# Performance work log

Hardware: AMD Instinct MI355X
Metric: run time of the kernel (lower is better)

Reference implementation:

```python
import jax, jax.numpy as jnp
import numpy as np

B, SEQ, PRED, N, PATCH, STRIDE = 4, 720, 720, 64, 16, 8
DM, EL = 256, 2
PNUM = (PRED + SEQ - PATCH) // STRIDE + 2  # 180
EPS = 1e-5


def _gelu(x):
    return jax.nn.gelu(x, approximate=False)  # torch nn.GELU default (erf)


def _ln(x, w, b):
    mu = x.mean(-1, keepdims=True)
    var = ((x - mu) ** 2).mean(-1, keepdims=True)
    return (x - mu) / jnp.sqrt(var + EPS) * w + b


def _pos_emb(n, d):
    pos = np.arange(n)[:, None].astype(np.float32)
    div = np.exp(np.arange(0, d, 2).astype(np.float32) * (-np.log(10000.0) / d))
    pe = np.zeros((n, d), np.float32)
    pe[:, 0::2] = np.sin(pos * div)
    pe[:, 1::2] = np.cos(pos * div)
    return jnp.asarray(pe)


def _patch_embed(x, emb_w):
    # x: [B, N, L]; ReplicationPad1d((0, STRIDE)) then unfold(patch_len, stride)
    xp = jnp.concatenate([x, jnp.repeat(x[..., -1:], STRIDE, axis=-1)], axis=-1)
    npatch = (xp.shape[-1] - PATCH) // STRIDE + 1
    idx = jnp.arange(npatch)[:, None] * STRIDE + jnp.arange(PATCH)[None, :]
    patches = xp[..., idx]  # [B, N, npatch, PATCH]
    emb = jnp.einsum('bnpl,ld->bnpd', patches, emb_w) + _pos_emb(npatch, DM)
    return emb.reshape(-1, npatch, DM)  # [B*N, npatch, DM]


def _temp_mix(x, w1, b1, w2, b2, nw, nb):
    # Pnum independent Linear(DM,DM)->GELU->Linear(DM,DM), residual + LayerNorm
    h = _gelu(jnp.einsum('bpd,pde->bpe', x, w1) + b1[None])
    o = jnp.einsum('bpd,pde->bpe', h, w2) + b2[None]
    return _ln(o + x, nw, nb)


def _chan_mix(x, w1, b1, w2, b2, nw, nb):
    # DM independent Linear(PNUM,PNUM)->GELU->Linear(PNUM,PNUM), residual + LayerNorm
    h = _gelu(jnp.einsum('bpd,dpq->bqd', x, w1) + b1.T[None])
    o = jnp.einsum('bpd,dpq->bqd', h, w2) + b2.T[None]
    return _ln(o + x, nw, nb)


def _s_correction(x, x_pre):
    xf = jnp.fft.rfft(x, axis=1, norm='ortho')
    pf = jnp.fft.rfft(x_pre, axis=1, norm='ortho')
    xi = jnp.maximum(jnp.fft.irfft(xf * jnp.conj(xf), axis=1), 0.0)
    pi = jnp.maximum(jnp.fft.irfft(pf * jnp.conj(pf), axis=1), 0.0)
    alpha = (xi * pi).sum(1, keepdims=True) / ((pi * pi).sum(1, keepdims=True) + 0.001)
    return jnp.sqrt(alpha)


def _forward(history_data, future_data, revin_w, revin_b, pred_w, pred_b, emb_w,
             ln_w, ln_b, comb_w, comb_b, head_w, head_b,
             tmd_w1, tmd_b1, tmd_w2, tmd_b2, tmd_nw, tmd_nb,
             cmd_w1, cmd_b1, cmd_w2, cmd_b2, cmd_nw, cmd_nb,
             tmu_w1, tmu_b1, tmu_w2, tmu_b2, tmu_nw, tmu_nb,
             cmu_w1, cmu_b1, cmu_w2, cmu_b2, cmu_nw, cmu_nb):
    x0 = history_data[:, :, :, 0]  # [B, SEQ, N]
    mean = x0.mean(1, keepdims=True)
    stdev = jnp.sqrt(x0.var(1, keepdims=True) + EPS)  # unbiased=False
    xn = (x0 - mean) / stdev * revin_w + revin_b  # RevIN norm (affine)
    x = jnp.einsum('bln,lt->bnt', xn, pred_w) + pred_b  # predict_linear on [B,N,SEQ]
    xi = _patch_embed(x, emb_w)  # [B*N, PNUM, DM]
    x_old = _patch_embed(jnp.transpose(x0, (0, 2, 1)), emb_w)  # [B*N, P_old, DM]
    x_all = jnp.zeros(xi.shape + (EL,), xi.dtype)
    for li in range(EL):
        xud = _temp_mix(xi, tmd_w1[li], tmd_b1[li], tmd_w2[li], tmd_b2[li], tmd_nw[li], tmd_nb[li])
        xud = _chan_mix(xud, cmd_w1[li], cmd_b1[li], cmd_w2[li], cmd_b2[li], cmd_nw[li], cmd_nb[li])
        for j in range(li, -1, -1):
            xud = _temp_mix(xud, tmu_w1[j], tmu_b1[j], tmu_w2[j], tmu_b2[j], tmu_nw[j], tmu_nb[j])
            xud = _chan_mix(xud, cmu_w1[j], cmu_b1[j], cmu_w2[j], cmu_b2[j], cmu_nw[j], cmu_nb[j])
        # faithful to original: inner loop shadows `i`, so the write index is always 0
        x_all = x_all.at[:, :, :, 0].set(xud)
    xc = jnp.einsum('bpde,e->bpd', x_all, comb_w) + comb_b  # comb: Linear(EL, 1)
    p_old = x_old.shape[1]
    xc = _s_correction(_ln(x_old, ln_w, ln_b), _ln(xc[:, :p_old, :], ln_w, ln_b)) * xc
    xr = xc.reshape(-1, N, PNUM, DM).transpose(0, 1, 3, 2)  # [B, N, DM, PNUM]
    out = xr.reshape(xr.shape[0], N, DM * PNUM) @ head_w + head_b  # Flatten_Head -> [B, N, PRED]
    out = jnp.transpose(out, (0, 2, 1))  # [B, PRED, N]
    out = (out - revin_b) / (revin_w + EPS * EPS) * stdev + mean  # RevIN denorm
    return out[:, -PRED:, :][..., None]  # [B, PRED, N, 1]


def setup_inputs() -> dict:
    key = jax.random.key(0)
    ks = iter(jax.random.split(key, 64))
    f = lambda shape, s=0.02: s * jax.random.normal(next(ks), shape, jnp.float32)
    inp = dict(
        history_data=jax.random.normal(next(ks), (B, SEQ, N, 1), jnp.float32),
        future_data=jax.random.normal(next(ks), (B, PRED, N, 1), jnp.float32),
        batch_seen=0, epoch=0, train=0,
        revin_w=jnp.ones((N,), jnp.float32), revin_b=jnp.zeros((N,), jnp.float32),
        pred_w=f((SEQ, SEQ + PRED)), pred_b=jnp.zeros((SEQ + PRED,), jnp.float32),
        emb_w=f((PATCH, DM)),
        ln_w=jnp.ones((DM,), jnp.float32), ln_b=jnp.zeros((DM,), jnp.float32),
        comb_w=f((EL,), 0.5), comb_b=jnp.zeros((), jnp.float32),
        head_w=f((DM * PNUM, PRED), 0.005), head_b=jnp.zeros((PRED,), jnp.float32),
    )
    for pre in ('tmd', 'tmu'):
        inp[pre + '_w1'] = f((EL, PNUM, DM, DM)); inp[pre + '_b1'] = jnp.zeros((EL, PNUM, DM), jnp.float32)
        inp[pre + '_w2'] = f((EL, PNUM, DM, DM)); inp[pre + '_b2'] = jnp.zeros((EL, PNUM, DM), jnp.float32)
        inp[pre + '_nw'] = jnp.ones((EL, DM), jnp.float32); inp[pre + '_nb'] = jnp.zeros((EL, DM), jnp.float32)
    for pre in ('cmd', 'cmu'):
        inp[pre + '_w1'] = f((EL, DM, PNUM, PNUM)); inp[pre + '_b1'] = jnp.zeros((EL, DM, PNUM), jnp.float32)
        inp[pre + '_w2'] = f((EL, DM, PNUM, PNUM)); inp[pre + '_b2'] = jnp.zeros((EL, DM, PNUM), jnp.float32)
        inp[pre + '_nw'] = jnp.ones((EL, DM), jnp.float32); inp[pre + '_nb'] = jnp.zeros((EL, DM), jnp.float32)
    return inp


def reference(history_data, future_data, revin_w, revin_b, pred_w, pred_b, emb_w,
              ln_w, ln_b, comb_w, comb_b, head_w, head_b,
              tmd_w1, tmd_b1, tmd_w2, tmd_b2, tmd_nw, tmd_nb,
              cmd_w1, cmd_b1, cmd_w2, cmd_b2, cmd_nw, cmd_nb,
              tmu_w1, tmu_b1, tmu_w2, tmu_b2, tmu_nw, tmu_nb,
              cmu_w1, cmu_b1, cmu_w2, cmu_b2, cmu_nw, cmu_nb,
              batch_seen, epoch, train):
    return _forward(history_data, future_data, revin_w, revin_b, pred_w, pred_b, emb_w,
                    ln_w, ln_b, comb_w, comb_b, head_w, head_b,
                    tmd_w1, tmd_b1, tmd_w2, tmd_b2, tmd_nw, tmd_nb,
                    cmd_w1, cmd_b1, cmd_w2, cmd_b2, cmd_nw, cmd_nb,
                    tmu_w1, tmu_b1, tmu_w2, tmu_b2, tmu_nw, tmu_nb,
                    cmu_w1, cmu_b1, cmu_w2, cmu_b2, cmu_nw, cmu_nb)
```

## Files before the change

### kernel.cpp

```cpp
#include <hip/hip_runtime.h>
#include <cstdint>
#include <cstddef>

namespace {

constexpr int SEQ_ = 720;
constexpr int N_ = 64;
constexpr int T_ = 1440;
constexpr int P_ = 180;
constexpr int PO_ = 90;
constexpr int D_ = 256;
constexpr int PD_ = P_ * D_;
constexpr float EPS_ = 1e-5f;

typedef __attribute__((ext_vector_type(8))) short bf16x8;
typedef __attribute__((ext_vector_type(4))) float f32x4;
typedef __attribute__((ext_vector_type(4))) unsigned short u16x4;

__device__ __forceinline__ float gelu_exact(float x) {
  return 0.5f * x * (1.0f + erff(x * 0.70710678118654752f));
}

__device__ __forceinline__ unsigned short f2bf(float x) {
  unsigned int u = __float_as_uint(x);
  u += 0x7FFFu + ((u >> 16) & 1u);
  return (unsigned short)(u >> 16);
}

__device__ __forceinline__ float bf2f(unsigned short h) {
  return __uint_as_float(((unsigned int)h) << 16);
}

__global__ __launch_bounds__(256) void revin_stats_kernel(
    const float* __restrict__ hist, const float* __restrict__ rw,
    const float* __restrict__ rb, float* __restrict__ meanA,
    float* __restrict__ stdevA, float* __restrict__ sA, float* __restrict__ sB) {
  int b = blockIdx.x;
  int tid = threadIdx.x;
  int n = tid & 63, c = tid >> 6;
  float s = 0.f, s2 = 0.f;
  for (int l = c; l < SEQ_; l += 4) {
    float v = hist[(size_t)(b * SEQ_ + l) * N_ + n];
    s += v; s2 += v * v;
  }
  __shared__ float rs[4][64], rq[4][64];
  rs[c][n] = s; rq[c][n] = s2;
  __syncthreads();
  if (tid < 64) {
    float S = rs[0][tid] + rs[1][tid] + rs[2][tid] + rs[3][tid];
    float Q = rq[0][tid] + rq[1][tid] + rq[2][tid] + rq[3][tid];
    float mu = S * (1.f / (float)SEQ_);
    float var = Q * (1.f / (float)SEQ_) - mu * mu;
    float sd = sqrtf(var + EPS_);
    int bn = b * 64 + tid;
    meanA[bn] = mu; stdevA[bn] = sd;
    float a = rw[tid] / sd;
    sA[bn] = a;
    sB[bn] = rb[tid] - mu * a;
  }
}

__global__ __launch_bounds__(256) void pred_kernel(
    const float* __restrict__ hist, const float* __restrict__ predw,
    const float* __restrict__ predb, const float* __restrict__ sA,
    const float* __restrict__ sB, float* __restrict__ xbuf) {
  int b = blockIdx.y;
  int t = blockIdx.x * 32 + (threadIdx.x & 31);
  int ng = threadIdx.x >> 5;
  const float* hb = hist + (size_t)b * SEQ_ * N_ + ng * 8;
  float acc[8] = {0.f,0.f,0.f,0.f,0.f,0.f,0.f,0.f};
  float wsum = 0.f;
  #pragma unroll 4
  for (int l = 0; l < SEQ_; l++) {
    float w = predw[(size_t)l * T_ + t];
    float4 h0 = *reinterpret_cast<const float4*>(hb + (size_t)l * N_);
    float4 h1 = *reinterpret_cast<const float4*>(hb + (size_t)l * N_ + 4);
    acc[0] += h0.x * w; acc[1] += h0.y * w; acc[2] += h0.z * w; acc[3] += h0.w * w;
    acc[4] += h1.x * w; acc[5] += h1.y * w; acc[6] += h1.z * w; acc[7] += h1.w * w;
    wsum += w;
  }
  float pb = predb[t];
  #pragma unroll
  for (int q = 0; q < 8; q++) {
    int bn = b * 64 + ng * 8 + q;
    xbuf[(size_t)bn * T_ + t] = sA[bn] * acc[q] + sB[bn] * wsum + pb;
  }
}

__global__ __launch_bounds__(256) void embed_kernel(
    const float* __restrict__ src, const float* __restrict__ embw,
    unsigned short* __restrict__ dst, int mode,
    float* __restrict__ muX, float* __restrict__ rsX) {
  __shared__ float Es[16 * 256];
  __shared__ float Ss[128];
  __shared__ float pS[15][4], pQ[15][4];
  int bn = blockIdx.y;
  int p0 = blockIdx.x * 15;
  int tid = threadIdx.x;
  for (int i = tid; i < 16 * 256; i += 256) Es[i] = embw[i];
  if (tid < 128) {
    int t = p0 * 8 + tid;
    float v;
    if (mode == 0) {
      int tc = t < T_ ? t : (T_ - 1);
      v = src[(size_t)bn * T_ + tc];
    } else {
      int tc = t < SEQ_ ? t : (SEQ_ - 1);
      int b = bn >> 6, n = bn & 63;
      v = src[(size_t)(b * SEQ_ + tc) * N_ + n];
    }
    Ss[tid] = v;
  }
  __syncthreads();
  int np = (mode == 0) ? P_ : PO_;
  float dv = expf(-0.035977892078032f * (float)(tid & ~1));
  int w = tid >> 6, l = tid & 63;
  for (int pi = 0; pi < 15; pi++) {
    int p = p0 + pi;
    float acc = 0.f;
    #pragma unroll
    for (int k = 0; k < 16; k++) acc += Ss[pi * 8 + k] * Es[k * 256 + tid];
    float ang = (float)p * dv;
    float pe = (tid & 1) ? cosf(ang) : sinf(ang);
    float ov = acc + pe;
    dst[((size_t)bn * np + p) * D_ + tid] = f2bf(ov);
    if (mode == 1) {
      float s = ov, q = ov * ov;
      #pragma unroll
      for (int off = 32; off > 0; off >>= 1) { s += __shfl_xor(s, off); q += __shfl_xor(q, off); }
      if (l == 0) { pS[pi][w] = s; pQ[pi][w] = q; }
    }
  }
  if (mode == 1) {
    __syncthreads();
    if (tid < 15) {
      float S = pS[tid][0] + pS[tid][1] + pS[tid][2] + pS[tid][3];
      float Q = pQ[tid][0] + pQ[tid][1] + pQ[tid][2] + pQ[tid][3];
      float mu = S * (1.f / 256.f);
      int idx = bn * 90 + p0 + tid;
      muX[idx] = mu;
      rsX[idx] = rsqrtf(Q * (1.f / 256.f) - mu * mu + EPS_);
    }
  }
}

struct TileInfo {
  const float* Wg; unsigned short* Og;
  int K, Nn, Kp, k0, n0;
};

__device__ __forceinline__ TileInfo decode_tile(
    int bid,
    const float* t0, const float* t1, const float* t2, const float* t3,
    const float* t4, const float* t5,
    const float* c0, const float* c1, const float* c2, const float* c3,
    const float* c4p, const float* c5, const float* hw,
    unsigned short* WtAll, unsigned short* WcAll, unsigned short* WhAll) {
  TileInfo ti;
  int tk, tn;
  if (bid < 17280) {
    int tt = bid / 2880, rem = bid - tt * 2880;
    int g = rem >> 4, tile = rem & 15;
    const float* s = t0;
    if (tt == 1) s = t1; else if (tt == 2) s = t2; else if (tt == 3) s = t3;
    else if (tt == 4) s = t4; else if (tt == 5) s = t5;
    ti.Wg = s + (size_t)g * 65536;
    ti.Og = WtAll + (size_t)tt * 11796480 + (size_t)g * 65536;
    ti.K = 256; ti.Nn = 256; ti.Kp = 256; tk = tile >> 2; tn = tile & 3;
  } else if (bid < 31104) {
    int b2 = bid - 17280;
    int tt = b2 / 2304, rem = b2 - tt * 2304;
    int g = rem / 9, tile = rem - g * 9;
    const float* s = c0;
    if (tt == 1) s = c1; else if (tt == 2) s = c2; else if (tt == 3) s = c3;
    else if (tt == 4) s = c4p; else if (tt == 5) s = c5;
    ti.Wg = s + (size_t)g * 32400;
    ti.Og = WcAll + (size_t)tt * 9437184 + (size_t)g * 36864;
    ti.K = 180; ti.Nn = 180; ti.Kp = 192; tk = tile / 3; tn = tile - (tile / 3) * 3;
  } else {
    int b2 = bid - 31104;
    ti.Wg = hw; ti.Og = WhAll;
    ti.K = 46080; ti.Nn = 720; ti.Kp = 46080; tk = b2 / 12; tn = b2 - (b2 / 12) * 12;
  }
  ti.k0 = tk * 64; ti.n0 = tn * 64;
  return ti;
}

__global__ __launch_bounds__(256) void convT_all_kernel(
    const float* t0, const float* t1, const float* t2, const float* t3,
    const float* t4, const float* t5,
    const float* c0, const float* c1, const float* c2, const float* c3,
    const float* c4p, const float* c5,
    const float* hw,
    unsigned short* WtAll, unsigned short* WcAll, unsigned short* WhAll,
    int tbase, int tcount) {
  __shared__ float Ts[2][64][65];
  int tid = threadIdx.x;
  int kr = tid >> 4, nc = (tid & 15) * 4;
  int G = gridDim.x;
  int tend = tbase + tcount;

  auto do_load = [&](const TileInfo& ti, float4* r) {
    #pragma unroll
    for (int i = 0; i < 4; i++) {
      int k = ti.k0 + kr + i * 16;
      float4 v = make_float4(0.f, 0.f, 0.f, 0.f);
      if (k < ti.K) {
        int n = ti.n0 + nc;
        if (n + 3 < ti.Nn) {
          v = *reinterpret_cast<const float4*>(ti.Wg + (size_t)k * ti.Nn + n);
        } else {
          if (n + 0 < ti.Nn) v.x = ti.Wg[(size_t)k * ti.Nn + n + 0];
          if (n + 1 < ti.Nn) v.y = ti.Wg[(size_t)k * ti.Nn + n + 1];
          if (n + 2 < ti.Nn) v.z = ti.Wg[(size_t)k * ti.Nn + n + 2];
          if (n + 3 < ti.Nn) v.w = ti.Wg[(size_t)k * ti.Nn + n + 3];
        }
      }
      r[i] = v;
    }
  };

  auto do_write = [&](const float4* r, int b) {
    #pragma unroll
    for (int i = 0; i < 4; i++) {
      Ts[b][kr + i * 16][nc + 0] = r[i].x;
      Ts[b][kr + i * 16][nc + 1] = r[i].y;
      Ts[b][kr + i * 16][nc + 2] = r[i].z;
      Ts[b][kr + i * 16][nc + 3] = r[i].w;
    }
  };

  auto do_store = [&](const TileInfo& ti, int b) {
    #pragma unroll
    for (int it = 0; it < 2; it++) {
      int nr = (tid >> 3) + it * 32;
      int kc = (tid & 7) * 8;
      unsigned int tmp[4];
      #pragma unroll
      for (int j = 0; j < 4; j++) {
        unsigned int lo = f2bf(Ts[b][kc + 2 * j][nr]);
        unsigned int hi = f2bf(Ts[b][kc + 2 * j + 1][nr]);
        tmp[j] = lo | (hi << 16);
      }
      uint4 vv; vv.x = tmp[0]; vv.y = tmp[1]; vv.z = tmp[2]; vv.w = tmp[3];
      *reinterpret_cast<uint4*>(ti.Og + (size_t)(ti.n0 + nr) * ti.Kp + ti.k0 + kc) = vv;
    }
  };

#define DECODE(tt) decode_tile((tt), t0,t1,t2,t3,t4,t5, c0,c1,c2,c3,c4p,c5, hw, WtAll, WcAll, WhAll)

  int t = tbase + blockIdx.x;
  if (t >= tend) return;

  float4 rA[4], rB[4];
  TileInfo i0 = DECODE(t);
  do_load(i0, rA);
  bool v1 = (t + G < tend);
  TileInfo i1 = v1 ? DECODE(t + G) : i0;
  if (v1) do_load(i1, rB);
  do_write(rA, 0);
  bool v2 = (t + 2 * G < tend);
  TileInfo i2 = v2 ? DECODE(t + 2 * G) : i0;
  if (v2) do_load(i2, rA);
  __syncthreads();

  while (true) {
    if (v1) do_write(rB, 1);
    {
      bool v3 = (t + 3 * G < tend);
      TileInfo i3 = i2;
      if (v3) { i3 = DECODE(t + 3 * G); do_load(i3, rB); }
      do_store(i0, 0);
      __syncthreads();
      t += G;
      if (!v1) return;
      i0 = i1; i1 = i2; i2 = i3; v1 = v2; v2 = v3;
    }
    if (v1) do_write(rA, 0);
    {
      bool v3 = (t + 3 * G < tend);
      TileInfo i3 = i2;
      if (v3) { i3 = DECODE(t + 3 * G); do_load(i3, rA); }
      do_store(i0, 1);
      __syncthreads();
      t += G;
      if (!v1) return;
      i0 = i1; i1 = i2; i2 = i3; v1 = v2; v2 = v3;
    }
  }
#undef DECODE
}

__global__ __launch_bounds__(256, 2) void temp_mfma_kernel(
    const unsigned short* __restrict__ X, unsigned short* __restrict__ Y,
    const unsigned short* __restrict__ W1t, const float* __restrict__ B1,
    const unsigned short* __restrict__ W2t, const float* __restrict__ B2,
    const float* __restrict__ NW, const float* __restrict__ NB) {
  __shared__ __align__(16) short Xs[64 * 256];
  __shared__ __align__(16) short Hs[64 * 256];
  __shared__ float partS[64][4];
  __shared__ float partQ[64][4];
  int lin = (blockIdx.x & 7) * 90 + (blockIdx.x >> 3);
  int p = lin >> 2;
  int m0 = (lin & 3) << 6;
  int tid = threadIdx.x;
  int w = tid >> 6, l = tid & 63;
  int lr = l & 15, lq = l >> 4;

  const unsigned short* Xblk = X + (size_t)m0 * PD_ + (size_t)p * D_;
  for (int i = tid; i < 64 * 32; i += 256) {
    int r = i >> 5, c8 = (i & 31) << 3;
    uint4 v = *reinterpret_cast<const uint4*>(Xblk + (size_t)r * PD_ + c8);
    *reinterpret_cast<uint4*>(&Xs[r * 256 + (c8 ^ ((r & 7) << 3))]) = v;
  }
  __syncthreads();

  int n0w = w << 6;
  f32x4 zero4 = {0.f, 0.f, 0.f, 0.f};
  f32x4 acc[4][4];
  #pragma unroll
  for (int a = 0; a < 4; a++)
    #pragma unroll
    for (int b = 0; b < 4; b++) acc[a][b] = zero4;

  const unsigned short* W1p = W1t + (size_t)p * 65536;
  {
    bf16x8 bhc[4], bhn[4];
    #pragma unroll
    for (int nf = 0; nf < 4; nf++)
      bhc[nf] = *reinterpret_cast<const bf16x8*>(W1p + (size_t)(n0w + nf * 16 + lr) * 256 + lq * 8);
    for (int ks = 0; ks < 8; ks++) {
      int kb = ks * 32 + lq * 8;
      bf16x8 af[4];
      #pragma unroll
      for (int mf = 0; mf < 4; mf++) {
        int r = mf * 16 + lr;
        af[mf] = *reinterpret_cast<const bf16x8*>(&Xs[r * 256 + (kb ^ ((r & 7) << 3))]);
      }
      if (ks < 7) {
        #pragma unroll
        for (int nf = 0; nf < 4; nf++)
          bhn[nf] = *reinterpret_cast<const bf16x8*>(W1p + (size_t)(n0w + nf * 16 + lr) * 256 + kb + 32);
      }
      #pragma unroll
      for (int mf = 0; mf < 4; mf++)
        #pragma unroll
        for (int nf = 0; nf < 4; nf++)
          acc[mf][nf] = __builtin_amdgcn_mfma_f32_16x16x32_bf16(af[mf], bhc[nf], acc[mf][nf], 0, 0, 0);
      if (ks < 7) {
        #pragma unroll
        for (int nf = 0; nf < 4; nf++) bhc[nf] = bhn[nf];
      }
    }
  }

  #pragma unroll
  for (int nf = 0; nf < 4; nf++) {
    int n = n0w + nf * 16 + lr;
    float bias = B1[p * 256 + n];
    #pragma unroll
    for (int mf = 0; mf < 4; mf++)
      #pragma unroll
      for (int rg = 0; rg < 4; rg++) {
        int r = mf * 16 + lq * 4 + rg;
        Hs[r * 256 + (n ^ ((r & 7) << 3))] =
            (short)f2bf(gelu_exact(acc[mf][nf][rg] + bias));
      }
  }
  __syncthreads();

  #pragma unroll
  for (int a = 0; a < 4; a++)
    #pragma unroll
    for (int b = 0; b < 4; b++) acc[a][b] = zero4;
  const unsigned short* W2p = W2t + (size_t)p * 65536;
  {
    bf16x8 bhc[4], bhn[4];
    #pragma unroll
    for (int nf = 0; nf < 4; nf++)
      bhc[nf] = *reinterpret_cast<const bf16x8*>(W2p + (size_t)(n0w + nf * 16 + lr) * 256 + lq * 8);
    for (int ks = 0; ks < 8; ks++) {
      int kb = ks * 32 + lq * 8;
      bf16x8 af[4];
      #pragma unroll
      for (int mf = 0; mf < 4; mf++) {
        int r = mf * 16 + lr;
        af[mf] = *reinterpret_cast<const bf16x8*>(&Hs[r * 256 + (kb ^ ((r & 7) << 3))]);
      }
      if (ks < 7) {
        #pragma unroll
        for (int nf = 0; nf < 4; nf++)
          bhn[nf] = *reinterpret_cast<const bf16x8*>(W2p + (size_t)(n0w + nf * 16 + lr) * 256 + kb + 32);
      }
      #pragma unroll
      for (int mf = 0; mf < 4; mf++)
        #pragma unroll
        for (int nf = 0; nf < 4; nf++)
          acc[mf][nf] = __builtin_amdgcn_mfma_f32_16x16x32_bf16(af[mf], bhc[nf], acc[mf][nf], 0, 0, 0);
      if (ks < 7) {
        #pragma unroll
        for (int nf = 0; nf < 4; nf++) bhc[nf] = bhn[nf];
      }
    }
  }

  float b2v[4], nwv[4], nbv[4];
  #pragma unroll
  for (int nf = 0; nf < 4; nf++) {
    int n = n0w + nf * 16 + lr;
    b2v[nf] = B2[p * 256 + n];
    nwv[nf] = NW[n];
    nbv[nf] = NB[n];
  }
  #pragma unroll
  for (int nf = 0; nf < 4; nf++) {
    int n = n0w + nf * 16 + lr;
    #pragma unroll
    for (int mf = 0; mf < 4; mf++)
      #pragma unroll
      for (int rg = 0; rg < 4; rg++) {
        int r = mf * 16 + lq * 4 + rg;
        float res = bf2f((unsigned short)Xs[r * 256 + (n ^ ((r & 7) << 3))]);
        acc[mf][nf][rg] += b2v[nf] + res;
      }
  }
  #pragma unroll
  for (int mf = 0; mf < 4; mf++)
    #pragma unroll
    for (int rg = 0; rg < 4; rg++) {
      float s = acc[mf][0][rg] + acc[mf][1][rg] + acc[mf][2][rg] + acc[mf][3][rg];
      float q = acc[mf][0][rg] * acc[mf][0][rg] + acc[mf][1][rg] * acc[mf][1][rg] +
                acc[mf][2][rg] * acc[mf][2][rg] + acc[mf][3][rg] * acc[mf][3][rg];
      #pragma unroll
      for (int off = 1; off < 16; off <<= 1) {
        s += __shfl_xor(s, off);
        q += __shfl_xor(q, off);
      }
      if (lr == 0) {
        int r = mf * 16 + lq * 4 + rg;
        partS[r][w] = s;
        partQ[r][w] = q;
      }
    }
  __syncthreads();
  #pragma unroll
  for (int mf = 0; mf < 4; mf++)
    #pragma unroll
    for (int rg = 0; rg < 4; rg++) {
      int r = mf * 16 + lq * 4 + rg;
      float S = partS[r][0] + partS[r][1] + partS[r][2] + partS[r][3];
      float Q = partQ[r][0] + partQ[r][1] + partQ[r][2] + partQ[r][3];
      float mu = S * (1.f / 256.f);
      float rstd = rsqrtf(Q * (1.f / 256.f) - mu * mu + EPS_);
      #pragma unroll
      for (int nf = 0; nf < 4; nf++) {
        int n = n0w + nf * 16 + lr;
        Hs[r * 256 + (n ^ ((r & 7) << 3))] =
            (short)f2bf((acc[mf][nf][rg] - mu) * rstd * nwv[nf] + nbv[nf]);
      }
    }
  __syncthreads();
  unsigned short* Yblk = Y + (size_t)m0 * PD_ + (size_t)p * D_;
  for (int i = tid; i < 64 * 32; i += 256) {
    int r = i >> 5, c8 = (i & 31) << 3;
    uint4 v = *reinterpret_cast<uint4*>(&Hs[r * 256 + (c8 ^ ((r & 7) << 3))]);
    *reinterpret_cast<uint4*>(Yblk + (size_t)r * PD_ + c8) = v;
  }
}

__global__ __launch_bounds__(256) void tr_AB_kernel(
    const unsigned short* __restrict__ A, unsigned short* __restrict__ B16) {
  __shared__ unsigned short T[32][184];
  int bn = blockIdx.y;
  int d0 = blockIdx.x * 32;
  int tid = threadIdx.x;
  int ld = tid & 31, pw = tid >> 5;
  for (int p = pw; p < 180; p += 8)
    T[ld][p] = A[((size_t)bn * 180 + p) * 256 + d0 + ld];
  __syncthreads();
  unsigned int* Bu = reinterpret_cast<unsigned int*>(B16);
  for (int i = tid; i < 32 * 96; i += 256) {
    int r = i / 96, jj = i - r * 96;
    int p0 = 2 * jj;
    unsigned int lo = (p0 < 180) ? (unsigned int)T[r][p0] : 0u;
    unsigned int hi = (p0 + 1 < 180) ? (unsigned int)T[r][p0 + 1] : 0u;
    Bu[((size_t)bn * 256 + d0 + r) * 96 + jj] = lo | (hi << 16);
  }
}

__global__ __launch_bounds__(256, 2) void chan_mfma_kernel(
    const unsigned short* __restrict__ Xb, unsigned short* __restrict__ Yb,
    const unsigned short* __restrict__ W1t, const float* __restrict__ B1,
    const unsigned short* __restrict__ W2t, const float* __restrict__ B2) {
  __shared__ __align__(16) short Xs[64 * 200];
  __shared__ __align__(16) short Hs[64 * 200];
  int lin = (blockIdx.x & 7) * 128 + (blockIdx.x >> 3);
  int d = lin >> 2;
  int m0 = (lin & 3) << 6;
  int tid = threadIdx.x;
  int w = tid >> 6, l = tid & 63;
  int lr = l & 15, lq = l >> 4;

  for (int i = tid; i < 64 * 24; i += 256) {
    int r = i / 24, c = i - r * 24;
    uint4 v = *reinterpret_cast<const uint4*>(
        Xb + ((size_t)(m0 + r) * 256 + d) * 192 + c * 8);
    *reinterpret_cast<uint4*>(&Xs[r * 200 + c * 8]) = v;
  }
  __syncthreads();

  int n0w = w * 48;
  f32x4 zero4 = {0.f, 0.f, 0.f, 0.f};
  f32x4 acc[4][3];
  #pragma unroll
  for (int a = 0; a < 4; a++)
    #pragma unroll
    for (int b = 0; b < 3; b++) acc[a][b] = zero4;

  const unsigned short* W1p = W1t + (size_t)d * (192 * 192);
  {
    bf16x8 bhc[3], bhn[3];
    #pragma unroll
    for (int nf = 0; nf < 3; nf++)
      bhc[nf] = *reinterpret_cast<const bf16x8*>(W1p + (size_t)(n0w + nf * 16 + lr) * 192 + lq * 8);
    for (int ks = 0; ks < 6; ks++) {
      int kb = ks * 32 + lq * 8;
      bf16x8 af[4];
      #pragma unroll
      for (int mf = 0; mf < 4; mf++)
        af[mf] = *reinterpret_cast<const bf16x8*>(&Xs[(mf * 16 + lr) * 200 + kb]);
      if (ks < 5) {
        #pragma unroll
        for (int nf = 0; nf < 3; nf++)
          bhn[nf] = *reinterpret_cast<const bf16x8*>(W1p + (size_t)(n0w + nf * 16 + lr) * 192 + kb + 32);
      }
      #pragma unroll
      for (int mf = 0; mf < 4; mf++)
        #pragma unroll
        for (int nf = 0; nf < 3; nf++)
          acc[mf][nf] = __builtin_amdgcn_mfma_f32_16x16x32_bf16(af[mf], bhc[nf], acc[mf][nf], 0, 0, 0);
      if (ks < 5) {
        #pragma unroll
        for (int nf = 0; nf < 3; nf++) bhc[nf] = bhn[nf];
      }
    }
  }

  #pragma unroll
  for (int nf = 0; nf < 3; nf++) {
    int n = n0w + nf * 16 + lr;
    bool valid = n < 180;
    float bias = valid ? B1[d * 180 + n] : 0.f;
    #pragma unroll
    for (int mf = 0; mf < 4; mf++)
      #pragma unroll
      for (int rg = 0; rg < 4; rg++) {
        int r = mf * 16 + lq * 4 + rg;
        float h = valid ? gelu_exact(acc[mf][nf][rg] + bias) : 0.f;
        Hs[r * 200 + n] = (short)f2bf(h);
      }
  }
  __syncthreads();

  #pragma unroll
  for (int a = 0; a < 4; a++)
    #pragma unroll
    for (int b = 0; b < 3; b++) acc[a][b] = zero4;
  const unsigned short* W2p = W2t + (size_t)d * (192 * 192);
  {
    bf16x8 bhc[3], bhn[3];
    #pragma unroll
    for (int nf = 0; nf < 3; nf++)
      bhc[nf] = *reinterpret_cast<const bf16x8*>(W2p + (size_t)(n0w + nf * 16 + lr) * 192 + lq * 8);
    for (int ks = 0; ks < 6; ks++) {
      int kb = ks * 32 + lq * 8;
      bf16x8 af[4];
      #pragma unroll
      for (int mf = 0; mf < 4; mf++)
        af[mf] = *reinterpret_cast<const bf16x8*>(&Hs[(mf * 16 + lr) * 200 + kb]);
      if (ks < 5) {
        #pragma unroll
        for (int nf = 0; nf < 3; nf++)
          bhn[nf] = *reinterpret_cast<const bf16x8*>(W2p + (size_t)(n0w + nf * 16 + lr) * 192 + kb + 32);
      }
      #pragma unroll
      for (int mf = 0; mf < 4; mf++)
        #pragma unroll
        for (int nf = 0; nf < 3; nf++)
          acc[mf][nf] = __builtin_amdgcn_mfma_f32_16x16x32_bf16(af[mf], bhc[nf], acc[mf][nf], 0, 0, 0);
      if (ks < 5) {
        #pragma unroll
        for (int nf = 0; nf < 3; nf++) bhc[nf] = bhn[nf];
      }
    }
  }

  #pragma unroll
  for (int nf = 0; nf < 3; nf++) {
    int n = n0w + nf * 16 + lr;
    if (n < 180) {
      float b2v = B2[d * 180 + n];
      #pragma unroll
      for (int mf = 0; mf < 4; mf++)
        #pragma unroll
        for (int rg = 0; rg < 4; rg++) {
          int r = mf * 16 + lq * 4 + rg;
          float res = bf2f((unsigned short)Xs[r * 200 + n]);
          Yb[((size_t)(m0 + r) * 256 + d) * 180 + n] = f2bf(acc[mf][nf][rg] + b2v + res);
        }
    }
  }
}

__global__ __launch_bounds__(256) void trLN_kernel(
    const unsigned short* __restrict__ Bsrc, unsigned short* __restrict__ A,
    const float* __restrict__ nw, const float* __restrict__ nb,
    const float* __restrict__ cw, const float* __restrict__ cb, int useComb,
    float* __restrict__ muP, float* __restrict__ rsP) {
  __shared__ float Tl[16][260];
  int bn = blockIdx.y;
  int p0 = blockIdx.x * 16;
  int tid = threadIdx.x;
  int j = tid & 15, db = tid >> 4;
  #pragma unroll 4
  for (int it = 0; it < 16; ++it) {
    int dd = it * 16 + db;
    float v = 0.f;
    if (p0 + j < 180)
      v = bf2f(Bsrc[((size_t)(bn * 256) + dd) * 180 + p0 + j]);
    Tl[j][dd] = v;
  }
  __syncthreads();
  int w = tid >> 6, l = tid & 63;
  float scale = 1.f, shift = 0.f;
  if (useComb) { scale = cw[0]; shift = cb[0]; }
  float4 w4 = *reinterpret_cast<const float4*>(nw + l * 4);
  float4 b4 = *reinterpret_cast<const float4*>(nb + l * 4);
  #pragma unroll
  for (int rr = 0; rr < 4; ++rr) {
    int row = w * 4 + rr;
    int p = p0 + row;
    float4 v = *reinterpret_cast<const float4*>(&Tl[row][l * 4]);
    float s = v.x + v.y + v.z + v.w;
    float s2 = v.x*v.x + v.y*v.y + v.z*v.z + v.w*v.w;
    #pragma unroll
    for (int off = 32; off > 0; off >>= 1) { s += __shfl_xor(s, off); s2 += __shfl_xor(s2, off); }
    float mu = s * (1.f/256.f);
    float rstd = rsqrtf(s2 * (1.f/256.f) - mu * mu + EPS_);
    if (p < 180) {
      float o0 = ((v.x - mu) * rstd * w4.x + b4.x) * scale + shift;
      float o1 = ((v.y - mu) * rstd * w4.y + b4.y) * scale + shift;
      float o2 = ((v.z - mu) * rstd * w4.z + b4.z) * scale + shift;
      float o3 = ((v.w - mu) * rstd * w4.w + b4.w) * scale + shift;
      unsigned int w0 = (unsigned int)f2bf(o0) | ((unsigned int)f2bf(o1) << 16);
      unsigned int w1 = (unsigned int)f2bf(o2) | ((unsigned int)f2bf(o3) << 16);
      unsigned int* dst = reinterpret_cast<unsigned int*>(
          A + ((size_t)bn * 180 + p) * 256 + l * 4);
      dst[0] = w0; dst[1] = w1;
      if (useComb && p < 90) {
        float so = o0 + o1 + o2 + o3;
        float qo = o0*o0 + o1*o1 + o2*o2 + o3*o3;
        #pragma unroll
        for (int off = 32; off > 0; off >>= 1) { so += __shfl_xor(so, off); qo += __shfl_xor(qo, off); }
        if (l == 0) {
          float muo = so * (1.f/256.f);
          muP[bn * 90 + p] = muo;
          rsP[bn * 90 + p] = rsqrtf(qo * (1.f/256.f) - muo * muo + EPS_);
        }
      }
    }
  }
}

__global__ __launch_bounds__(128, 1) void autocorr_kernel(
    const unsigned short* __restrict__ xoldB, const unsigned short* __restrict__ xcB,
    const float* __restrict__ muX, const float* __restrict__ rsX,
    const float* __restrict__ muP, const float* __restrict__ rsP,
    const float* __restrict__ lnw, const float* __restrict__ lnb,
    float* __restrict__ sqa) {
  __shared__ float PI[46][64];
  __shared__ float RED[2][2][64];
  int bn = blockIdx.x >> 2;
  int tid = threadIdx.x;
  int dl = tid & 63;
  int half = tid >> 6;
  int j0 = half * 23;
  int d = ((blockIdx.x & 3) << 6) + dl;
  float w = lnw[d], bb = lnb[d];
  float v[90], wr[90];

  {
    const unsigned short* col = xcB + (size_t)bn * PD_ + d;
    const float* m = muP + bn * 90;
    const float* rs = rsP + bn * 90;
    #pragma unroll
    for (int p = 0; p < 90; p++)
      v[p] = (bf2f(col[(size_t)p * D_]) - m[p]) * rs[p] * w + bb;
    #pragma unroll
    for (int p = 0; p < 90; p++)
      wr[p] = (half == 0) ? v[p] : v[(p + 23) % 90];
  }
  float den = 0.f;
  #pragma unroll 1
  for (int jt = 0; jt < 24; jt += 4) {
    float c0 = 0.f, c1 = 0.f, c2 = 0.f, c3 = 0.f;
    #pragma unroll
    for (int mm = 0; mm < 90; mm++) {
      float vm = v[mm];
      c0 += vm * wr[mm];
      c1 += vm * ((mm + 1 < 90) ? wr[mm + 1] : wr[mm - 89]);
      c2 += vm * ((mm + 2 < 90) ? wr[mm + 2] : wr[mm - 88]);
      c3 += vm * ((mm + 3 < 90) ? wr[mm + 3] : wr[mm - 87]);
    }
    float cq[4] = {c0, c1, c2, c3};
    #pragma unroll
    for (int q = 0; q < 4; q++) {
      if (jt + q < 23) {
        int lag = j0 + jt + q;
        float piv = fmaxf(cq[q] * 0.10540925533894598f, 0.f);
        PI[lag][dl] = piv;
        float wgt = (lag == 0 || lag == 45) ? 1.f : 2.f;
        den += wgt * piv * piv;
      }
    }
    float t0 = wr[0], t1 = wr[1], t2 = wr[2], t3 = wr[3];
    #pragma unroll
    for (int mm = 0; mm < 86; mm++) wr[mm] = wr[mm + 4];
    wr[86] = t0; wr[87] = t1; wr[88] = t2; wr[89] = t3;
  }

  {
    const unsigned short* col = xoldB + (size_t)bn * (PO_ * D_) + d;
    const float* m = muX + bn * 90;
    const float* rs = rsX + bn * 90;
    #pragma unroll
    for (int p = 0; p < 90; p++)
      v[p] = (bf2f(col[(size_t)p * D_]) - m[p]) * rs[p] * w + bb;
    #pragma unroll
    for (int p = 0; p < 90; p++)
      wr[p] = (half == 0) ? v[p] : v[(p + 23) % 90];
  }
  float num = 0.f;
  #pragma unroll 1
  for (int jt = 0; jt < 24; jt += 4) {
    float c0 = 0.f, c1 = 0.f, c2 = 0.f, c3 = 0.f;
    #pragma unroll
    for (int mm = 0; mm < 90; mm++) {
      float vm = v[mm];
      c0 += vm * wr[mm];
      c1 += vm * ((mm + 1 < 90) ? wr[mm + 1] : wr[mm - 89]);
      c2 += vm * ((mm + 2 < 90) ? wr[mm + 2] : wr[mm - 88]);
      c3 += vm * ((mm + 3 < 90) ? wr[mm + 3] : wr[mm - 87]);
    }
    float cq[4] = {c0, c1, c2, c3};
    #pragma unroll
    for (int q = 0; q < 4; q++) {
      if (jt + q < 23) {
        int lag = j0 + jt + q;
        float xi = fmaxf(cq[q] * 0.10540925533894598f, 0.f);
        float wgt = (lag == 0 || lag == 45) ? 1.f : 2.f;
        num += wgt * xi * PI[lag][dl];
      }
    }
    float t0 = wr[0], t1 = wr[1], t2 = wr[2], t3 = wr[3];
    #pragma unroll
    for (int mm = 0; mm < 86; mm++) wr[mm] = wr[mm + 4];
    wr[86] = t0; wr[87] = t1; wr[88] = t2; wr[89] = t3;
  }
  RED[0][half][dl] = den;
  RED[1][half][dl] = num;
  __syncthreads();
  if (half == 0) {
    float Dn = RED[0][0][dl] + RED[0][1][dl];
    float Nm = RED[1][0][dl] + RED[1][1][dl];
    sqa[bn * D_ + d] = sqrtf(Nm / (Dn + 0.001f));
  }
}

__global__ __launch_bounds__(256) void scale_tr_kernel(
    const unsigned short* __restrict__ Xc, const float* __restrict__ sqa,
    unsigned short* __restrict__ Xt) {
  __shared__ float Ts[32][33];
  int bn = blockIdx.y;
  int pt = blockIdx.x % 6, dt = blockIdx.x / 6;
  int p0 = pt * 32, d0 = dt * 32;
  int tid = threadIdx.x;
  {
    int pr = tid >> 3, c4 = (tid & 7) * 4;
    if (p0 + pr < 180) {
      u16x4 h = *reinterpret_cast<const u16x4*>(
          Xc + ((size_t)bn * 180 + p0 + pr) * 256 + d0 + c4);
      Ts[pr][c4]   = bf2f(h[0]); Ts[pr][c4+1] = bf2f(h[1]);
      Ts[pr][c4+2] = bf2f(h[2]); Ts[pr][c4+3] = bf2f(h[3]);
    }
  }
  __syncthreads();
  {
    int dr = tid >> 3, p4 = (tid & 7) * 4;
    float sc = sqa[bn * D_ + d0 + dr];
    #pragma unroll
    for (int i = 0; i < 4; i++) {
      int pp = p0 + p4 + i;
      if (pp < 180)
        Xt[(size_t)bn * PD_ + (size_t)(d0 + dr) * 180 + pp] = f2bf(Ts[p4 + i][dr] * sc);
    }
  }
}

__global__ __launch_bounds__(256, 2) void head_mfma_kernel(
    const unsigned short* __restrict__ A, const unsigned short* __restrict__ Bw,
    float* __restrict__ P) {
  __shared__ float Rs[64][65];
  int lin = (blockIdx.x & 7) * 96 + (blockIdx.x >> 3);
  int ks = lin / 48;
  int rem = lin - ks * 48;
  int mt = rem & 3, nt = rem >> 2;
  int m0 = mt << 6, n0 = nt << 6;
  int tid = threadIdx.x;
  int w = tid >> 6, l = tid & 63;
  int lr = l & 15, lq = l >> 4;
  f32x4 zero4 = {0.f, 0.f, 0.f, 0.f};
  f32x4 acc[4][4];
  #pragma unroll
  for (int a = 0; a < 4; a++)
    #pragma unroll
    for (int b = 0; b < 4; b++) acc[a][b] = zero4;

  size_t kbase = (size_t)ks * 2880;
  bf16x8 afc[4], bhc[4], afn[4], bhn[4];
  {
    size_t kb = kbase + (size_t)w * 32 + lq * 8;
    #pragma unroll
    for (int mf = 0; mf < 4; mf++)
      afc[mf] = *reinterpret_cast<const bf16x8*>(A + (size_t)(m0 + mf * 16 + lr) * 46080 + kb);
    #pragma unroll
    for (int nf = 0; nf < 4; nf++)
      bhc[nf] = *reinterpret_cast<const bf16x8*>(Bw + (size_t)(n0 + nf * 16 + lr) * 46080 + kb);
  }
  for (int s = w; s < 90; s += 4) {
    int sn = s + 4;
    if (sn < 90) {
      size_t kb = kbase + (size_t)sn * 32 + lq * 8;
      #pragma unroll
      for (int mf = 0; mf < 4; mf++)
        afn[mf] = *reinterpret_cast<const bf16x8*>(A + (size_t)(m0 + mf * 16 + lr) * 46080 + kb);
      #pragma unroll
      for (int nf = 0; nf < 4; nf++)
        bhn[nf] = *reinterpret_cast<const bf16x8*>(Bw + (size_t)(n0 + nf * 16 + lr) * 46080 + kb);
    }
    #pragma unroll
    for (int mf = 0; mf < 4; mf++)
      #pragma unroll
      for (int nf = 0; nf < 4; nf++)
        acc[mf][nf] = __builtin_amdgcn_mfma_f32_16x16x32_bf16(afc[mf], bhc[nf], acc[mf][nf], 0, 0, 0);
    if (sn < 90) {
      #pragma unroll
      for (int mf = 0; mf < 4; mf++) afc[mf] = afn[mf];
      #pragma unroll
      for (int nf = 0; nf < 4; nf++) bhc[nf] = bhn[nf];
    }
  }
  for (int ww = 0; ww < 4; ww++) {
    if (w == ww) {
      #pragma unroll
      for (int mf = 0; mf < 4; mf++)
        #pragma unroll
        for (int nf = 0; nf < 4; nf++)
          #pragma unroll
          for (int rg = 0; rg < 4; rg++) {
            int r = mf * 16 + lq * 4 + rg, c = nf * 16 + lr;
            if (ww == 0) Rs[r][c] = acc[mf][nf][rg];
            else Rs[r][c] += acc[mf][nf][rg];
          }
    }
    __syncthreads();
  }
  for (int i = tid; i < 64 * 64; i += 256) {
    int r = i >> 6, c = i & 63;
    int n = n0 + c;
    if (n < 720)
      P[((size_t)ks * 256 + m0 + r) * 720 + n] = Rs[r][c];
  }
}

__global__ __launch_bounds__(256) void final_kernel(
    const float* __restrict__ P, const float* __restrict__ hb,
    const float* __restrict__ rw, const float* __restrict__ rb,
    const float* __restrict__ meanA, const float* __restrict__ stdevA,
    float* __restrict__ out) {
  int gid = blockIdx.x * 256 + threadIdx.x;
  int bn = gid / 720, t = gid - bn * 720;
  float s = 0.f;
  #pragma unroll
  for (int ks = 0; ks < 16; ks++) s += P[(size_t)ks * 184320 + gid];
  s += hb[t];
  int b = bn >> 6, n = bn & 63;
  float val = (s - rb[n]) / (rw[n] + 1e-10f) * stdevA[bn] + meanA[bn];
  out[((size_t)(b * 720 + t)) * 64 + n] = val;
}

}

extern "C" void kernel_launch(void* const* d_in, const int* in_sizes, int n_in,
                              void* d_out, int out_size, void* d_ws, size_t ws_size,
                              hipStream_t stream) {
  (void)in_sizes; (void)n_in; (void)out_size; (void)ws_size;
  const float* hist   = (const float*)d_in[0];
  const float* revw   = (const float*)d_in[5];
  const float* revb   = (const float*)d_in[6];
  const float* predw  = (const float*)d_in[7];
  const float* predb  = (const float*)d_in[8];
  const float* embw   = (const float*)d_in[9];
  const float* lnw    = (const float*)d_in[10];
  const float* lnb    = (const float*)d_in[11];
  const float* combw  = (const float*)d_in[12];
  const float* combb  = (const float*)d_in[13];
  const float* headw  = (const float*)d_in[14];
  const float* headb  = (const float*)d_in[15];
  const float* tmd_w1 = (const float*)d_in[16];
  const float* tmd_b1 = (const float*)d_in[17];
  const float* tmd_w2 = (const float*)d_in[18];
  const float* tmd_b2 = (const float*)d_in[19];
  const float* tmd_nw = (const float*)d_in[20];
  const float* tmd_nb = (const float*)d_in[21];
  const float* tmu_w1 = (const float*)d_in[22];
  const float* tmu_b1 = (const float*)d_in[23];
  const float* tmu_w2 = (const float*)d_in[24];
  const float* tmu_b2 = (const float*)d_in[25];
  const float* tmu_nw = (const float*)d_in[26];
  const float* tmu_nb = (const float*)d_in[27];
  const float* cmd_w1 = (const float*)d_in[28];
  const float* cmd_b1 = (const float*)d_in[29];
  const float* cmd_w2 = (const float*)d_in[30];
  const float* cmd_b2 = (const float*)d_in[31];
  const float* cmd_nw = (const float*)d_in[32];
  const float* cmd_nb = (const float*)d_in[33];
  const float* cmu_w1 = (const float*)d_in[34];
  const float* cmu_b1 = (const float*)d_in[35];
  const float* cmu_w2 = (const float*)d_in[36];
  const float* cmu_b2 = (const float*)d_in[37];
  const float* cmu_nw = (const float*)d_in[38];
  const float* cmu_nb = (const float*)d_in[39];

  float* ws = (float*)d_ws;
  float* meanA  = ws;
  float* stdevA = meanA + 256;
  float* sA     = stdevA + 256;
  float* sB     = sA + 256;
  float* muX    = sB + 256;
  float* rsX    = muX + 23040;
  float* muP    = rsX + 23040;
  float* rsP    = muP + 23040;
  float* sqa    = rsP + 23040;
  float* xbuf   = sqa + 65536;
  unsigned short* xoldB = (unsigned short*)(xbuf + 368640);
  unsigned short* A0    = xoldB + 5898240;
  unsigned short* A1    = A0 + 11796480;
  unsigned short* B16   = A1 + 11796480;
  unsigned short* Yb    = B16 + 12582912;
  float* part           = (float*)(Yb + 11796480);
  unsigned short* Xtb   = (unsigned short*)(part + 2949120);
  unsigned short* WtAll = Xtb + 11796480;
  unsigned short* WcAll = WtAll + 70778880;
  unsigned short* WhAll = WcAll + 56623104;

  constexpr int TW = 180 * 256 * 256, TB = 180 * 256;
  constexpr int CW = 256 * 180 * 180, CB = 256 * 180;
  constexpr size_t TSTR = 11796480, CSTR = 9437184;

  convT_all_kernel<<<2048, 256, 0, stream>>>(
      tmd_w1 + TW, tmd_w2 + TW, tmu_w1 + TW, tmu_w2 + TW, tmu_w1, tmu_w2,
      cmd_w1 + CW, cmd_w2 + CW, cmu_w1 + CW, cmu_w2 + CW, cmu_w1, cmu_w2,
      headw, WtAll, WcAll, WhAll, 0, 17280);
  convT_all_kernel<<<2048, 256, 0, stream>>>(
      tmd_w1 + TW, tmd_w2 + TW, tmu_w1 + TW, tmu_w2 + TW, tmu_w1, tmu_w2,
      cmd_w1 + CW, cmd_w2 + CW, cmu_w1 + CW, cmu_w2 + CW, cmu_w1, cmu_w2,
      headw, WtAll, WcAll, WhAll, 17280, 13824);
  convT_all_kernel<<<2048, 256, 0, stream>>>(
      tmd_w1 + TW, tmd_w2 + TW, tmu_w1 + TW, tmu_w2 + TW, tmu_w1, tmu_w2,
      cmd_w1 + CW, cmd_w2 + CW, cmu_w1 + CW, cmu_w2 + CW, cmu_w1, cmu_w2,
      headw, WtAll, WcAll, WhAll, 31104, 8640);

  revin_stats_kernel<<<4, 256, 0, stream>>>(hist, revw, revb, meanA, stdevA, sA, sB);
  pred_kernel<<<dim3(45, 4), 256, 0, stream>>>(hist, predw, predb, sA, sB, xbuf);
  embed_kernel<<<dim3(12, 256), 256, 0, stream>>>(xbuf, embw, A0, 0, nullptr, nullptr);
  embed_kernel<<<dim3(6, 256), 256, 0, stream>>>(hist, embw, xoldB, 1, muX, rsX);

  const float* tB1[3] = {tmd_b1 + TB, tmu_b1 + TB, tmu_b1};
  const float* tB2[3] = {tmd_b2 + TB, tmu_b2 + TB, tmu_b2};
  const float* tNW[3] = {tmd_nw + 256, tmu_nw + 256, tmu_nw};
  const float* tNB[3] = {tmd_nb + 256, tmu_nb + 256, tmu_nb};
  const float* cB1[3] = {cmd_b1 + CB, cmu_b1 + CB, cmu_b1};
  const float* cB2[3] = {cmd_b2 + CB, cmu_b2 + CB, cmu_b2};
  const float* cNW[3] = {cmd_nw + 256, cmu_nw + 256, cmu_nw};
  const float* cNB[3] = {cmd_nb + 256, cmu_nb + 256, cmu_nb};

  for (int li = 0; li < 3; li++) {
    temp_mfma_kernel<<<720, 256, 0, stream>>>(
        A0, A1, WtAll + (size_t)(2 * li) * TSTR, tB1[li],
        WtAll + (size_t)(2 * li + 1) * TSTR, tB2[li], tNW[li], tNB[li]);
    tr_AB_kernel<<<dim3(8, 256), 256, 0, stream>>>(A1, B16);
    chan_mfma_kernel<<<1024, 256, 0, stream>>>(
        B16, Yb, WcAll + (size_t)(2 * li) * CSTR, cB1[li],
        WcAll + (size_t)(2 * li + 1) * CSTR, cB2[li]);
    trLN_kernel<<<dim3(12, 256), 256, 0, stream>>>(Yb, A0, cNW[li], cNB[li],
                                                   combw, combb, li == 2 ? 1 : 0,
                                                   muP, rsP);
  }

  autocorr_kernel<<<1024, 128, 0, stream>>>(xoldB, A0, muX, rsX, muP, rsP, lnw, lnb, sqa);
  scale_tr_kernel<<<dim3(48, 256), 256, 0, stream>>>(A0, sqa, Xtb);
  head_mfma_kernel<<<768, 256, 0, stream>>>(Xtb, WhAll, part);
  final_kernel<<<720, 256, 0, stream>>>(part, headb, revw, revb, meanA, stdevA, (float*)d_out);
}
```

Baseline: 1.203 ms.

## Reuse the input LDS tile for hidden activations and merge weight-conversion launches

```diff
diff --git a/kernel.cpp b/kernel.cpp
--- a/kernel.cpp
+++ b/kernel.cpp
@@ -12,6 +12,7 @@
 constexpr int D_ = 256;
 constexpr int PD_ = P_ * D_;
 constexpr float EPS_ = 1e-5f;
+constexpr int NTILE_ = 39744;
 
 typedef __attribute__((ext_vector_type(8))) short bf16x8;
 typedef __attribute__((ext_vector_type(4))) float f32x4;
@@ -291,13 +292,12 @@
 #undef DECODE
 }
 
-__global__ __launch_bounds__(256, 2) void temp_mfma_kernel(
+__global__ __launch_bounds__(256, 3) void temp_mfma_kernel(
     const unsigned short* __restrict__ X, unsigned short* __restrict__ Y,
     const unsigned short* __restrict__ W1t, const float* __restrict__ B1,
     const unsigned short* __restrict__ W2t, const float* __restrict__ B2,
     const float* __restrict__ NW, const float* __restrict__ NB) {
   __shared__ __align__(16) short Xs[64 * 256];
-  __shared__ __align__(16) short Hs[64 * 256];
   __shared__ float partS[64][4];
   __shared__ float partQ[64][4];
   int lin = (blockIdx.x & 7) * 90 + (blockIdx.x >> 3);
@@ -353,6 +353,7 @@
       }
     }
   }
+  __syncthreads();
 
   #pragma unroll
   for (int nf = 0; nf < 4; nf++) {
@@ -363,7 +364,7 @@
       #pragma unroll
       for (int rg = 0; rg < 4; rg++) {
         int r = mf * 16 + lq * 4 + rg;
-        Hs[r * 256 + (n ^ ((r & 7) << 3))] =
+        Xs[r * 256 + (n ^ ((r & 7) << 3))] =
             (short)f2bf(gelu_exact(acc[mf][nf][rg] + bias));
       }
   }
@@ -385,7 +386,7 @@
       #pragma unroll
       for (int mf = 0; mf < 4; mf++) {
         int r = mf * 16 + lr;
-        af[mf] = *reinterpret_cast<const bf16x8*>(&Hs[r * 256 + (kb ^ ((r & 7) << 3))]);
+        af[mf] = *reinterpret_cast<const bf16x8*>(&Xs[r * 256 + (kb ^ ((r & 7) << 3))]);
       }
       if (ks < 7) {
         #pragma unroll
@@ -420,7 +421,7 @@
       #pragma unroll
       for (int rg = 0; rg < 4; rg++) {
         int r = mf * 16 + lq * 4 + rg;
-        float res = bf2f((unsigned short)Xs[r * 256 + (n ^ ((r & 7) << 3))]);
+        float res = bf2f(Xblk[(size_t)r * PD_ + n]);
         acc[mf][nf][rg] += b2v[nf] + res;
       }
   }
@@ -455,7 +456,7 @@
       #pragma unroll
       for (int nf = 0; nf < 4; nf++) {
         int n = n0w + nf * 16 + lr;
-        Hs[r * 256 + (n ^ ((r & 7) << 3))] =
+        Xs[r * 256 + (n ^ ((r & 7) << 3))] =
             (short)f2bf((acc[mf][nf][rg] - mu) * rstd * nwv[nf] + nbv[nf]);
       }
     }
@@ -463,7 +464,7 @@
   unsigned short* Yblk = Y + (size_t)m0 * PD_ + (size_t)p * D_;
   for (int i = tid; i < 64 * 32; i += 256) {
     int r = i >> 5, c8 = (i & 31) << 3;
-    uint4 v = *reinterpret_cast<uint4*>(&Hs[r * 256 + (c8 ^ ((r & 7) << 3))]);
+    uint4 v = *reinterpret_cast<uint4*>(&Xs[r * 256 + (c8 ^ ((r & 7) << 3))]);
     *reinterpret_cast<uint4*>(Yblk + (size_t)r * PD_ + c8) = v;
   }
 }
@@ -488,12 +489,11 @@
   }
 }
 
-__global__ __launch_bounds__(256, 2) void chan_mfma_kernel(
+__global__ __launch_bounds__(256, 3) void chan_mfma_kernel(
     const unsigned short* __restrict__ Xb, unsigned short* __restrict__ Yb,
     const unsigned short* __restrict__ W1t, const float* __restrict__ B1,
     const unsigned short* __restrict__ W2t, const float* __restrict__ B2) {
   __shared__ __align__(16) short Xs[64 * 200];
-  __shared__ __align__(16) short Hs[64 * 200];
   int lin = (blockIdx.x & 7) * 128 + (blockIdx.x >> 3);
   int d = lin >> 2;
   int m0 = (lin & 3) << 6;
@@ -545,6 +545,7 @@
       }
     }
   }
+  __syncthreads();
 
   #pragma unroll
   for (int nf = 0; nf < 3; nf++) {
@@ -557,7 +558,7 @@
       for (int rg = 0; rg < 4; rg++) {
         int r = mf * 16 + lq * 4 + rg;
         float h = valid ? gelu_exact(acc[mf][nf][rg] + bias) : 0.f;
-        Hs[r * 200 + n] = (short)f2bf(h);
+        Xs[r * 200 + n] = (short)f2bf(h);
       }
   }
   __syncthreads();
@@ -577,7 +578,7 @@
       bf16x8 af[4];
       #pragma unroll
       for (int mf = 0; mf < 4; mf++)
-        af[mf] = *reinterpret_cast<const bf16x8*>(&Hs[(mf * 16 + lr) * 200 + kb]);
+        af[mf] = *reinterpret_cast<const bf16x8*>(&Xs[(mf * 16 + lr) * 200 + kb]);
       if (ks < 5) {
         #pragma unroll
         for (int nf = 0; nf < 3; nf++)
@@ -605,7 +606,7 @@
         #pragma unroll
         for (int rg = 0; rg < 4; rg++) {
           int r = mf * 16 + lq * 4 + rg;
-          float res = bf2f((unsigned short)Xs[r * 200 + n]);
+          float res = bf2f(Xb[((size_t)(m0 + r) * 256 + d) * 192 + n]);
           Yb[((size_t)(m0 + r) * 256 + d) * 180 + n] = f2bf(acc[mf][nf][rg] + b2v + res);
         }
     }
@@ -971,15 +972,7 @@
   convT_all_kernel<<<2048, 256, 0, stream>>>(
       tmd_w1 + TW, tmd_w2 + TW, tmu_w1 + TW, tmu_w2 + TW, tmu_w1, tmu_w2,
       cmd_w1 + CW, cmd_w2 + CW, cmu_w1 + CW, cmu_w2 + CW, cmu_w1, cmu_w2,
-      headw, WtAll, WcAll, WhAll, 0, 17280);
-  convT_all_kernel<<<2048, 256, 0, stream>>>(
-      tmd_w1 + TW, tmd_w2 + TW, tmu_w1 + TW, tmu_w2 + TW, tmu_w1, tmu_w2,
-      cmd_w1 + CW, cmd_w2 + CW, cmu_w1 + CW, cmu_w2 + CW, cmu_w1, cmu_w2,
-      headw, WtAll, WcAll, WhAll, 17280, 13824);
-  convT_all_kernel<<<2048, 256, 0, stream>>>(
-      tmd_w1 + TW, tmd_w2 + TW, tmu_w1 + TW, tmu_w2 + TW, tmu_w1, tmu_w2,
-      cmd_w1 + CW, cmd_w2 + CW, cmu_w1 + CW, cmu_w2 + CW, cmu_w1, cmu_w2,
-      headw, WtAll, WcAll, WhAll, 31104, 8640);
+      headw, WtAll, WcAll, WhAll, 0, NTILE_);
 
   revin_stats_kernel<<<4, 256, 0, stream>>>(hist, revw, revb, meanA, stdevA, sA, sB);
   pred_kernel<<<dim3(45, 4), 256, 0, stream>>>(hist, predw, predb, sA, sB, xbuf);
```

Measured after the change: 1.112 ms. 1.08x faster.
